# Performance work log

Hardware: AMD Instinct MI355X
Metric: run time of the kernel (lower is better)

Reference implementation:

```python
import jax, jax.numpy as jnp
import numpy as np
import math

B, S, D, H, DQ, DV = 8, 1024, 1024, 16, 64, 64

def _layernorm(x, gamma, beta, eps=1e-5):
    mu = jnp.mean(x, axis=-1, keepdims=True)
    var = jnp.var(x, axis=-1, keepdims=True)
    return (x - mu) * jax.lax.rsqrt(var + eps) * gamma + beta

def setup_inputs() -> dict:
    key = jax.random.key(0)
    ks = jax.random.split(key, 6)
    x = jax.random.normal(ks[0], (B, S, D), dtype=jnp.float32)
    seq_lens = jax.random.randint(ks[1], (B,), 1, S + 1, dtype=jnp.int32)  # min 1 avoids fully-masked rows
    scale = 0.02
    Wq = jax.random.normal(ks[2], (D, H * DQ), dtype=jnp.float32) * scale
    Wkv = jax.random.normal(ks[3], (D, H * (DQ + DV)), dtype=jnp.float32) * scale
    Wo = jax.random.normal(ks[4], (H * DV, D), dtype=jnp.float32) * scale
    return {
        'x': x, 'seq_lens': seq_lens,
        'Wq': Wq, 'bq': jnp.zeros((H * DQ,), jnp.float32),
        'Wkv': Wkv, 'bkv': jnp.zeros((H * (DQ + DV),), jnp.float32),
        'Wo': Wo, 'bo': jnp.zeros((D,), jnp.float32),
        'gamma': jnp.ones((D,), jnp.float32), 'beta': jnp.zeros((D,), jnp.float32),
    }

def reference(x, seq_lens, Wq, bq, Wkv, bkv, Wo, bo, gamma, beta):
    # Decoder self-attention branch: query == key_value sequence.
    resid = x
    xn = _layernorm(x, gamma, beta)
    q = (xn @ Wq + bq).reshape(B, S, H, DQ).transpose(0, 2, 1, 3)      # bhqd
    kv = xn @ Wkv + bkv
    k = kv[..., : H * DQ].reshape(B, S, H, DQ).transpose(0, 2, 1, 3)   # bhkd
    v = kv[..., H * DQ :].reshape(B, S, H, DV).transpose(0, 2, 1, 3)   # bhkd
    scores = jnp.einsum('bhqd,bhkd->bhqk', q, k) / math.sqrt(DQ)
    key_pos = jnp.arange(S)
    pad_mask = key_pos[None, None, None, :] < seq_lens[:, None, None, None]  # [B,1,1,S]
    causal = jnp.tril(jnp.ones((S, S), dtype=bool))[None, None]              # [1,1,S,S]
    mask = pad_mask & causal
    scores = jnp.where(mask, scores, -jnp.inf)
    attn = jax.nn.softmax(scores, axis=-1)
    out = jnp.einsum('bhqk,bhkd->bhqd', attn, v)
    out = out.transpose(0, 2, 1, 3).reshape(B, S, H * DV)
    return out @ Wo + bo + resid
```

## Files before the change

### kernel.cpp

```cpp
#include <hip/hip_runtime.h>
#include <stdint.h>

#define ND 1024

typedef uint16_t u16;
typedef __bf16 bf16_t;
typedef bf16_t bf16x8 __attribute__((ext_vector_type(8)));
typedef float  f32x4  __attribute__((ext_vector_type(4)));
typedef u16    u16x8  __attribute__((ext_vector_type(8)));
typedef u16    u16x4  __attribute__((ext_vector_type(4)));

__device__ __forceinline__ float bf2f(u16 b){
    uint32_t u = ((uint32_t)b) << 16; float f; __builtin_memcpy(&f, &u, 4); return f;
}
__device__ __forceinline__ u16 f2bf(float f){
    uint32_t u; __builtin_memcpy(&u, &f, 4);
    u += 0x7FFFu + ((u >> 16) & 1u);
    return (u16)(u >> 16);
}
__device__ __forceinline__ bool bf_mode(const void* gamma){
    return *reinterpret_cast<const uint32_t*>(gamma) == 0x3F803F80u;
}
__device__ __forceinline__ float loadv(const void* p, int idx, bool bf){
    return bf ? bf2f(reinterpret_cast<const u16*>(p)[idx])
              : reinterpret_cast<const float*>(p)[idx];
}
__device__ __forceinline__ void gload16(const u16* g, u16* l){
    __builtin_amdgcn_global_load_lds(
        (const __attribute__((address_space(1))) void*)g,
        (__attribute__((address_space(3))) void*)l, 16, 0, 0);
}

__global__ __launch_bounds__(256) void k_ln(const void* __restrict__ x,
                                            const void* __restrict__ gamma,
                                            const void* __restrict__ beta,
                                            u16* __restrict__ xn){
    const bool bf = bf_mode(gamma);
    const int lane = threadIdx.x & 63;
    const int row  = blockIdx.x * 4 + (threadIdx.x >> 6);
    const size_t base = (size_t)row * 1024;
    float v[16];
    if (bf){
        const u16* xp = reinterpret_cast<const u16*>(x) + base;
        #pragma unroll
        for (int j = 0; j < 4; j++){
            u16x4 t4 = *reinterpret_cast<const u16x4*>(xp + j*256 + lane*4);
            #pragma unroll
            for (int e = 0; e < 4; e++) v[j*4 + e] = bf2f(t4[e]);
        }
    } else {
        const float* xp = reinterpret_cast<const float*>(x) + base;
        #pragma unroll
        for (int j = 0; j < 4; j++){
            float4 t = *reinterpret_cast<const float4*>(xp + j*256 + lane*4);
            v[j*4+0] = t.x; v[j*4+1] = t.y; v[j*4+2] = t.z; v[j*4+3] = t.w;
        }
    }
    float s1 = 0.f, s2 = 0.f;
    #pragma unroll
    for (int e = 0; e < 16; e++){ s1 += v[e]; s2 += v[e]*v[e]; }
    #pragma unroll
    for (int off = 32; off; off >>= 1){
        s1 += __shfl_xor(s1, off);
        s2 += __shfl_xor(s2, off);
    }
    const float mu  = s1 * (1.0f / ND);
    const float var = s2 * (1.0f / ND) - mu * mu;
    const float rs  = rsqrtf(var + 1e-5f);
    #pragma unroll
    for (int j = 0; j < 4; j++){
        u16x4 o;
        #pragma unroll
        for (int e = 0; e < 4; e++){
            const int col = j*256 + lane*4 + e;
            o[e] = f2bf((v[j*4+e] - mu) * rs * loadv(gamma, col, bf) + loadv(beta, col, bf));
        }
        *reinterpret_cast<u16x4*>(xn + base + j*256 + lane*4) = o;
    }
}

__global__ __launch_bounds__(256) void k_wt(const void* __restrict__ W,
                                            const void* __restrict__ gamma,
                                            u16* __restrict__ WT, int Ncols){
    const bool bf = bf_mode(gamma);
    __shared__ float tile[32][33];
    const int n0 = blockIdx.x * 32, k0 = blockIdx.y * 32;
    const int tx = threadIdx.x & 31, ty = threadIdx.x >> 5;
    #pragma unroll
    for (int r = 0; r < 4; r++){
        int kk = ty + r * 8;
        tile[kk][tx] = loadv(W, (k0 + kk) * Ncols + n0 + tx, bf);
    }
    __syncthreads();
    #pragma unroll
    for (int r = 0; r < 4; r++){
        int nn = ty + r * 8;
        WT[(size_t)(n0 + nn) * 1024 + k0 + tx] = f2bf(tile[tx][nn]);
    }
}

__global__ __launch_bounds__(256) void k_gemmA(const u16* __restrict__ A,
                                               const u16* __restrict__ BT,
                                               const void* __restrict__ bias0,
                                               const void* __restrict__ bias1,
                                               const void* __restrict__ gamma,
                                               u16* __restrict__ Qo, u16* __restrict__ Ko,
                                               u16* __restrict__ Vo){
    const bool bf = bf_mode(gamma);
    __shared__ u16 Al[128 * 64];
    __shared__ u16 Bl[128 * 64];
    const int x8 = blockIdx.x & 7;
    const int r  = blockIdx.x >> 3;
    const int s  = r >> 6;
    const int t  = r & 63;
    const int bm = x8 * 8 + (t & 7);
    const int bn = s * 8 + (t >> 3);
    const int tid = threadIdx.x, lane = tid & 63, w = tid >> 6;
    const int wr = w >> 1, wc = w & 1;
    const int l15 = lane & 15, g = lane >> 4;
    const int xr = (l15 & 7) * 8;
    f32x4 acc[4][4];
    #pragma unroll
    for (int m = 0; m < 4; m++)
        #pragma unroll
        for (int n = 0; n < 4; n++) acc[m][n] = f32x4{0.f, 0.f, 0.f, 0.f};

    const u16* Ag = A  + (size_t)(bm * 128) * 1024;
    const u16* Bg = BT + (size_t)(bn * 128) * 1024;
    const int srow = tid >> 3, sslot = tid & 7;
    const int sswz = (sslot * 8) ^ ((srow & 7) * 8);

    for (int k0 = 0; k0 < 1024; k0 += 64){
        #pragma unroll
        for (int call = 0; call < 4; call++){
            const int row = srow + call * 32;
            const int c   = tid + call * 256;
            gload16(Ag + (size_t)row * 1024 + k0 + sswz, Al + c * 8);
            gload16(Bg + (size_t)row * 1024 + k0 + sswz, Bl + c * 8);
        }
        __syncthreads();
        #pragma unroll
        for (int kc = 0; kc < 2; kc++){
            bf16x8 af[4], bfr[4];
            #pragma unroll
            for (int m = 0; m < 4; m++){
                const int row = wr*64 + m*16 + l15;
                u16x8 t8 = *reinterpret_cast<const u16x8*>(&Al[row*64 + ((kc*32 + g*8) ^ xr)]);
                af[m] = __builtin_bit_cast(bf16x8, t8);
            }
            #pragma unroll
            for (int n = 0; n < 4; n++){
                const int row = wc*64 + n*16 + l15;
                u16x8 t8 = *reinterpret_cast<const u16x8*>(&Bl[row*64 + ((kc*32 + g*8) ^ xr)]);
                bfr[n] = __builtin_bit_cast(bf16x8, t8);
            }
            #pragma unroll
            for (int m = 0; m < 4; m++)
                #pragma unroll
                for (int n = 0; n < 4; n++)
                    acc[m][n] = __builtin_amdgcn_mfma_f32_16x16x32_bf16(af[m], bfr[n], acc[m][n], 0, 0, 0);
        }
        __syncthreads();
    }
    #pragma unroll
    for (int m = 0; m < 4; m++){
        const int grow = bm * 128 + wr * 64 + m * 16 + g * 4;
        #pragma unroll
        for (int n = 0; n < 4; n++){
            const int gcol = bn * 128 + wc * 64 + n * 16 + l15;
            #pragma unroll
            for (int rr4 = 0; rr4 < 4; rr4++){
                float val = acc[m][n][rr4];
                const int rr = grow + rr4;
                const int b = rr >> 10, ss = rr & 1023;
                if (gcol < 1024){
                    int h = gcol >> 6, d = gcol & 63;
                    val = (val + loadv(bias0, gcol, bf)) * 0.18033688011112042f;
                    Qo[((size_t)(b*16 + h) * 1024 + ss) * 64 + d] = f2bf(val);
                } else if (gcol < 2048){
                    int n2 = gcol - 1024, h = n2 >> 6, d = n2 & 63;
                    val += loadv(bias1, n2, bf);
                    Ko[((size_t)(b*16 + h) * 1024 + ss) * 64 + d] = f2bf(val);
                } else {
                    int n3 = gcol - 2048, h = n3 >> 6, d = n3 & 63;
                    val += loadv(bias1, gcol - 1024, bf);
                    Vo[((size_t)(b*16 + h) * 1024 + ss) * 64 + d] = f2bf(val);
                }
            }
        }
    }
}

__global__ __launch_bounds__(256) void k_gemmB(const u16* __restrict__ A,
                                               const u16* __restrict__ BT,
                                               const void* __restrict__ bias0,
                                               const void* __restrict__ xres,
                                               const void* __restrict__ gamma,
                                               float* __restrict__ outf){
    const bool bf = bf_mode(gamma);
    __shared__ u16 Al[128 * 64];
    __shared__ u16 Bl[128 * 64];
    const int x8 = blockIdx.x & 7;
    const int r  = blockIdx.x >> 3;
    const int bm = x8 * 8 + (r & 7);
    const int bn = r >> 3;
    const int tid = threadIdx.x, lane = tid & 63, w = tid >> 6;
    const int wr = w >> 1, wc = w & 1;
    const int l15 = lane & 15, g = lane >> 4;
    const int xr = (l15 & 7) * 8;
    f32x4 acc[4][4];
    #pragma unroll
    for (int m = 0; m < 4; m++)
        #pragma unroll
        for (int n = 0; n < 4; n++) acc[m][n] = f32x4{0.f, 0.f, 0.f, 0.f};

    const u16* Ag = A  + (size_t)(bm * 128) * 1024;
    const u16* Bg = BT + (size_t)(bn * 128) * 1024;
    const int srow = tid >> 3, sslot = tid & 7;
    const int sswz = (sslot * 8) ^ ((srow & 7) * 8);

    for (int k0 = 0; k0 < 1024; k0 += 64){
        #pragma unroll
        for (int call = 0; call < 4; call++){
            const int row = srow + call * 32;
            const int c   = tid + call * 256;
            gload16(Ag + (size_t)row * 1024 + k0 + sswz, Al + c * 8);
            gload16(Bg + (size_t)row * 1024 + k0 + sswz, Bl + c * 8);
        }
        __syncthreads();
        #pragma unroll
        for (int kc = 0; kc < 2; kc++){
            bf16x8 af[4], bfr[4];
            #pragma unroll
            for (int m = 0; m < 4; m++){
                const int row = wr*64 + m*16 + l15;
                u16x8 t8 = *reinterpret_cast<const u16x8*>(&Al[row*64 + ((kc*32 + g*8) ^ xr)]);
                af[m] = __builtin_bit_cast(bf16x8, t8);
            }
            #pragma unroll
            for (int n = 0; n < 4; n++){
                const int row = wc*64 + n*16 + l15;
                u16x8 t8 = *reinterpret_cast<const u16x8*>(&Bl[row*64 + ((kc*32 + g*8) ^ xr)]);
                bfr[n] = __builtin_bit_cast(bf16x8, t8);
            }
            #pragma unroll
            for (int m = 0; m < 4; m++)
                #pragma unroll
                for (int n = 0; n < 4; n++)
                    acc[m][n] = __builtin_amdgcn_mfma_f32_16x16x32_bf16(af[m], bfr[n], acc[m][n], 0, 0, 0);
        }
        __syncthreads();
    }
    #pragma unroll
    for (int m = 0; m < 4; m++){
        const int grow = bm * 128 + wr * 64 + m * 16 + g * 4;
        #pragma unroll
        for (int n = 0; n < 4; n++){
            const int gcol = bn * 128 + wc * 64 + n * 16 + l15;
            #pragma unroll
            for (int rr4 = 0; rr4 < 4; rr4++){
                float val = acc[m][n][rr4];
                const int rr = grow + rr4;
                val += loadv(bias0, gcol, bf);
                val += loadv(xres, (int)((size_t)rr * 1024 + gcol), bf);
                outf[(size_t)rr * 1024 + gcol] = val;
            }
        }
    }
}

__global__ __launch_bounds__(64, 4) void k_attn(const u16* __restrict__ Q,
                                                const u16* __restrict__ K,
                                                const u16* __restrict__ V,
                                                const int* __restrict__ seq_lens,
                                                u16* __restrict__ AO){
    __shared__ u16 Kl0[32 * 64], Kl1[32 * 64];
    __shared__ u16 Vt[64 * 32];
    __shared__ u16 Pl[32 * 32];
    const int bid = blockIdx.x;
    const int qb = 31 - (bid >> 7);
    const int bh = bid & 127;
    const int b = bh >> 4, h = bh & 15;
    const int lane = threadIdx.x;
    const int l15 = lane & 15, g = lane >> 4;
    const int seqlen = seq_lens[b];
    const int nkt = (min(qb * 32 + 31, seqlen - 1) >> 5) + 1;
    const size_t kvbase = (size_t)bh * 1024;

    bf16x8 qa[2][2];
    #pragma unroll
    for (int m = 0; m < 2; m++)
        #pragma unroll
        for (int kc = 0; kc < 2; kc++){
            const u16* qp = Q + (kvbase + qb*32 + m*16 + l15) * 64 + kc*32 + g*8;
            qa[m][kc] = __builtin_bit_cast(bf16x8, *reinterpret_cast<const u16x8*>(qp));
        }

    float m_run[2] = {-3.0e38f, -3.0e38f};
    float l_run[2] = {0.f, 0.f};
    f32x4 oacc[2][4];
    #pragma unroll
    for (int m = 0; m < 2; m++)
        #pragma unroll
        for (int nf = 0; nf < 4; nf++) oacc[m][nf] = f32x4{0.f, 0.f, 0.f, 0.f};

    const int srow8 = lane >> 3, sslot = lane & 7;
    u16x8 vr[4];

    auto stageK = [&](int kt, u16* dst){
        #pragma unroll
        for (int call = 0; call < 4; call++){
            const int row = srow8 + call * 8;
            const int c   = lane + call * 64;
            gload16(K + (kvbase + kt*32 + row) * 64 + ((sslot * 8) ^ ((row & 7) * 8)), dst + c * 8);
        }
    };
    auto vload = [&](int kt){
        #pragma unroll
        for (int j = 0; j < 4; j++){
            const int c = lane + j * 64;
            vr[j] = *reinterpret_cast<const u16x8*>(V + (kvbase + kt*32 + (c >> 3)) * 64 + (c & 7) * 8);
        }
    };
    auto vstore = [&](){
        #pragma unroll
        for (int j = 0; j < 4; j++){
            const int c = lane + j * 64, k = c >> 3, sl = c & 7;
            #pragma unroll
            for (int i = 0; i < 8; i++){
                const int d = sl * 8 + i;
                Vt[d * 32 + (((k >> 3) ^ ((d >> 3) & 3)) * 8) + (k & 7)] = vr[j][i];
            }
        }
    };

    stageK(0, Kl0); vload(0);
    u16* kcur = Kl0; u16* knext = Kl1;

    for (int kt = 0; kt < nkt; kt++){
        asm volatile("s_waitcnt vmcnt(0)" ::: "memory");
        __builtin_amdgcn_sched_barrier(0);
        vstore();
        const bool pre = (kt + 1 < nkt);
        if (pre){ stageK(kt + 1, knext); vload(kt + 1); }

        f32x4 sa[2][2];
        #pragma unroll
        for (int m = 0; m < 2; m++)
            #pragma unroll
            for (int n = 0; n < 2; n++) sa[m][n] = f32x4{0.f, 0.f, 0.f, 0.f};
        #pragma unroll
        for (int kc = 0; kc < 2; kc++){
            bf16x8 kf[2];
            #pragma unroll
            for (int n = 0; n < 2; n++){
                const int row = n*16 + l15;
                u16x8 t = *reinterpret_cast<const u16x8*>(&kcur[row*64 + ((kc*32 + g*8) ^ ((l15 & 7) * 8))]);
                kf[n] = __builtin_bit_cast(bf16x8, t);
            }
            #pragma unroll
            for (int m = 0; m < 2; m++)
                #pragma unroll
                for (int n = 0; n < 2; n++)
                    sa[m][n] = __builtin_amdgcn_mfma_f32_16x16x32_bf16(kf[n], qa[m][kc], sa[m][n], 0, 0, 0);
        }

        #pragma unroll
        for (int m = 0; m < 2; m++){
            const int q = qb*32 + m*16 + l15;
            const int klim = min(q, seqlen - 1);
            float p[8];
            float rm = -3.0e38f;
            #pragma unroll
            for (int n = 0; n < 2; n++)
                #pragma unroll
                for (int r4 = 0; r4 < 4; r4++){
                    const int k = kt*32 + n*16 + g*4 + r4;
                    float sv = sa[m][n][r4];
                    sv = (k <= klim) ? sv : -3.0e38f;
                    p[n*4 + r4] = sv;
                    rm = fmaxf(rm, sv);
                }
            rm = fmaxf(rm, __shfl_xor(rm, 16));
            rm = fmaxf(rm, __shfl_xor(rm, 32));
            const float mnew = fmaxf(m_run[m], rm);
            const float fac  = exp2f(m_run[m] - mnew);
            m_run[m] = mnew;
            float rs = 0.f;
            #pragma unroll
            for (int n = 0; n < 2; n++)
                #pragma unroll
                for (int r4 = 0; r4 < 4; r4++){
                    const float ev = exp2f(p[n*4 + r4] - mnew);
                    rs += ev;
                    const int ql = m*16 + l15;
                    const int k  = n*16 + g*4 + r4;
                    Pl[ql * 32 + (k ^ ((ql & 3) * 8))] = f2bf(ev);
                }
            rs += __shfl_xor(rs, 16);
            rs += __shfl_xor(rs, 32);
            l_run[m] = l_run[m] * fac + rs;
            #pragma unroll
            for (int r4 = 0; r4 < 4; r4++){
                const float facr = __shfl(fac, g*4 + r4, 16);
                #pragma unroll
                for (int nf = 0; nf < 4; nf++) oacc[m][nf][r4] *= facr;
            }
        }

        {
            bf16x8 pa[2], vf[4];
            #pragma unroll
            for (int m = 0; m < 2; m++){
                const int ql = m*16 + l15;
                u16x8 t = *reinterpret_cast<const u16x8*>(&Pl[ql * 32 + ((g ^ (ql & 3)) * 8)]);
                pa[m] = __builtin_bit_cast(bf16x8, t);
            }
            #pragma unroll
            for (int nf = 0; nf < 4; nf++){
                const int dv = nf*16 + l15;
                u16x8 t = *reinterpret_cast<const u16x8*>(&Vt[dv * 32 + ((g ^ ((dv >> 3) & 3)) * 8)]);
                vf[nf] = __builtin_bit_cast(bf16x8, t);
            }
            #pragma unroll
            for (int m = 0; m < 2; m++)
                #pragma unroll
                for (int nf = 0; nf < 4; nf++)
                    oacc[m][nf] = __builtin_amdgcn_mfma_f32_16x16x32_bf16(pa[m], vf[nf], oacc[m][nf], 0, 0, 0);
        }
        u16* tmp = kcur; kcur = knext; knext = tmp;
    }

    #pragma unroll
    for (int m = 0; m < 2; m++)
        #pragma unroll
        for (int r4 = 0; r4 < 4; r4++){
            const float lv  = __shfl(l_run[m], g*4 + r4, 16);
            const float inv = 1.0f / lv;
            const int sg = qb*32 + m*16 + g*4 + r4;
            #pragma unroll
            for (int nf = 0; nf < 4; nf++){
                const int col = h * 64 + nf * 16 + l15;
                AO[((size_t)b * 1024 + sg) * 1024 + col] = f2bf(oacc[m][nf][r4] * inv);
            }
        }
}

extern "C" void kernel_launch(void* const* d_in, const int* in_sizes, int n_in,
                              void* d_out, int out_size, void* d_ws, size_t ws_size,
                              hipStream_t stream){
    const int exp_sizes[10] = {8388608, 8, 1048576, 1024, 2097152, 2048, 1048576, 1024, 1024, 1024};
    if (n_in != 10) return;
    for (int i = 0; i < 10; i++) if (in_sizes[i] != exp_sizes[i]) return;

    const void* x     = d_in[0];
    const int*  slen  = (const int*)d_in[1];
    const void* Wq    = d_in[2];
    const void* bq    = d_in[3];
    const void* Wkv   = d_in[4];
    const void* bkv   = d_in[5];
    const void* Wo    = d_in[6];
    const void* bo    = d_in[7];
    const void* gamma = d_in[8];
    const void* beta  = d_in[9];

    u16* WTqkv = (u16*)d_ws;
    u16* WoT   = WTqkv + (size_t)3072 * 1024;
    u16* xn    = WoT   + (size_t)1024 * 1024;
    u16* Qb    = xn    + (size_t)8192 * 1024;
    u16* Kb    = Qb    + (size_t)8192 * 1024;
    u16* Vb    = Kb    + (size_t)8192 * 1024;
    u16* AOb   = xn;
    const size_t need = ((size_t)3072 + 1024 + 4 * 8192) * 1024 * 2;
    if (ws_size < need) return;

    k_ln<<<2048, 256, 0, stream>>>(x, gamma, beta, xn);
    k_wt<<<dim3(32, 32), 256, 0, stream>>>(Wq,  gamma, WTqkv, 1024);
    k_wt<<<dim3(64, 32), 256, 0, stream>>>(Wkv, gamma, WTqkv + (size_t)1024 * 1024, 2048);
    k_wt<<<dim3(32, 32), 256, 0, stream>>>(Wo,  gamma, WoT, 1024);
    k_gemmA<<<1536, 256, 0, stream>>>(xn, WTqkv, bq, bkv, gamma, Qb, Kb, Vb);
    k_attn<<<4096, 64, 0, stream>>>(Qb, Kb, Vb, slen, AOb);
    k_gemmB<<<512, 256, 0, stream>>>(AOb, WoT, bo, x, gamma, (float*)d_out);
}
```

Baseline: 230.3 us.

## Keep P in registers and read V via LDS transpose loads in attention

Drops the shared-memory round trip for the softmax probabilities: the exponentiated scores now stay in registers as bf16 MFMA operands, and the PV product switches to 16x16x16 MFMAs. V is staged with async global-to-LDS copies into a double buffer, replacing the register load plus scalar transposed stores, and is read back with ds_read_b64_tr_b16 transpose reads. This removes per-element LDS stores and an LDS barrier round trip. In exchange it issues twice as many smaller MFMAs, relies on inline assembly with a manual lgkmcnt wait, and uses more LDS per block.

```diff
diff --git a/kernel.cpp b/kernel.cpp
--- a/kernel.cpp
+++ b/kernel.cpp
@@ -9,6 +9,7 @@
 typedef float  f32x4  __attribute__((ext_vector_type(4)));
 typedef u16    u16x8  __attribute__((ext_vector_type(8)));
 typedef u16    u16x4  __attribute__((ext_vector_type(4)));
+typedef short  s16x4  __attribute__((ext_vector_type(4)));
 
 __device__ __forceinline__ float bf2f(u16 b){
     uint32_t u = ((uint32_t)b) << 16; float f; __builtin_memcpy(&f, &u, 4); return f;
@@ -29,6 +30,16 @@
     __builtin_amdgcn_global_load_lds(
         (const __attribute__((address_space(1))) void*)g,
         (__attribute__((address_space(3))) void*)l, 16, 0, 0);
+}
+__device__ __forceinline__ f32x4 mfma16(u16x4 a, u16x4 b, f32x4 c){
+#if __has_builtin(__builtin_amdgcn_mfma_f32_16x16x16bf16_1k)
+    return __builtin_amdgcn_mfma_f32_16x16x16bf16_1k(
+        __builtin_bit_cast(s16x4, a), __builtin_bit_cast(s16x4, b), c, 0, 0, 0);
+#else
+    f32x4 d = c;
+    asm("v_mfma_f32_16x16x16_bf16 %0, %1, %2, %0" : "+v"(d) : "v"(a), "v"(b));
+    return d;
+#endif
 }
 
 __global__ __launch_bounds__(256) void k_ln(const void* __restrict__ x,
@@ -275,8 +286,7 @@
                                                 const int* __restrict__ seq_lens,
                                                 u16* __restrict__ AO){
     __shared__ u16 Kl0[32 * 64], Kl1[32 * 64];
-    __shared__ u16 Vt[64 * 32];
-    __shared__ u16 Pl[32 * 32];
+    __shared__ u16 Vl0[32 * 64], Vl1[32 * 64];
     const int bid = blockIdx.x;
     const int qb = 31 - (bid >> 7);
     const int bh = bid & 127;
@@ -305,7 +315,6 @@
         for (int nf = 0; nf < 4; nf++) oacc[m][nf] = f32x4{0.f, 0.f, 0.f, 0.f};
 
     const int srow8 = lane >> 3, sslot = lane & 7;
-    u16x8 vr[4];
 
     auto stageK = [&](int kt, u16* dst){
         #pragma unroll
@@ -315,34 +324,26 @@
             gload16(K + (kvbase + kt*32 + row) * 64 + ((sslot * 8) ^ ((row & 7) * 8)), dst + c * 8);
         }
     };
-    auto vload = [&](int kt){
-        #pragma unroll
-        for (int j = 0; j < 4; j++){
-            const int c = lane + j * 64;
-            vr[j] = *reinterpret_cast<const u16x8*>(V + (kvbase + kt*32 + (c >> 3)) * 64 + (c & 7) * 8);
+    auto stageV = [&](int kt, u16* dst){
+        #pragma unroll
+        for (int call = 0; call < 4; call++){
+            const int c = lane + call * 64;
+            const int s = c >> 3;
+            const int k  = (s & 7) * 4 + ((c & 7) >> 1);
+            const int dv = (s >> 3) * 16 + ((c & 7) & 1) * 8;
+            gload16(V + (kvbase + kt*32 + k) * 64 + dv, dst + c * 8);
         }
     };
-    auto vstore = [&](){
-        #pragma unroll
-        for (int j = 0; j < 4; j++){
-            const int c = lane + j * 64, k = c >> 3, sl = c & 7;
-            #pragma unroll
-            for (int i = 0; i < 8; i++){
-                const int d = sl * 8 + i;
-                Vt[d * 32 + (((k >> 3) ^ ((d >> 3) & 3)) * 8) + (k & 7)] = vr[j][i];
-            }
-        }
-    };
-
-    stageK(0, Kl0); vload(0);
+
+    stageK(0, Kl0); stageV(0, Vl0);
     u16* kcur = Kl0; u16* knext = Kl1;
+    u16* vcur = Vl0; u16* vnext = Vl1;
 
     for (int kt = 0; kt < nkt; kt++){
         asm volatile("s_waitcnt vmcnt(0)" ::: "memory");
         __builtin_amdgcn_sched_barrier(0);
-        vstore();
         const bool pre = (kt + 1 < nkt);
-        if (pre){ stageK(kt + 1, knext); vload(kt + 1); }
+        if (pre){ stageK(kt + 1, knext); stageV(kt + 1, vnext); }
 
         f32x4 sa[2][2];
         #pragma unroll
@@ -365,11 +366,12 @@
                     sa[m][n] = __builtin_amdgcn_mfma_f32_16x16x32_bf16(kf[n], qa[m][kc], sa[m][n], 0, 0, 0);
         }
 
+        u16x4 pa[2][2];
         #pragma unroll
         for (int m = 0; m < 2; m++){
             const int q = qb*32 + m*16 + l15;
             const int klim = min(q, seqlen - 1);
-            float p[8];
+            float p[8], pe[8];
             float rm = -3.0e38f;
             #pragma unroll
             for (int n = 0; n < 2; n++)
@@ -388,15 +390,15 @@
             m_run[m] = mnew;
             float rs = 0.f;
             #pragma unroll
-            for (int n = 0; n < 2; n++)
-                #pragma unroll
-                for (int r4 = 0; r4 < 4; r4++){
-                    const float ev = exp2f(p[n*4 + r4] - mnew);
-                    rs += ev;
-                    const int ql = m*16 + l15;
-                    const int k  = n*16 + g*4 + r4;
-                    Pl[ql * 32 + (k ^ ((ql & 3) * 8))] = f2bf(ev);
-                }
+            for (int e = 0; e < 8; e++){
+                pe[e] = exp2f(p[e] - mnew);
+                rs += pe[e];
+            }
+            #pragma unroll
+            for (int j = 0; j < 4; j++){
+                pa[m][0][j] = f2bf(pe[j]);
+                pa[m][1][j] = f2bf(pe[4 + j]);
+            }
             rs += __shfl_xor(rs, 16);
             rs += __shfl_xor(rs, 32);
             l_run[m] = l_run[m] * fac + rs;
@@ -409,28 +411,32 @@
         }
 
         {
-            bf16x8 pa[2], vf[4];
-            #pragma unroll
-            for (int m = 0; m < 2; m++){
-                const int ql = m*16 + l15;
-                u16x8 t = *reinterpret_cast<const u16x8*>(&Pl[ql * 32 + ((g ^ (ql & 3)) * 8)]);
-                pa[m] = __builtin_bit_cast(bf16x8, t);
-            }
-            #pragma unroll
-            for (int nf = 0; nf < 4; nf++){
-                const int dv = nf*16 + l15;
-                u16x8 t = *reinterpret_cast<const u16x8*>(&Vt[dv * 32 + ((g ^ ((dv >> 3) & 3)) * 8)]);
-                vf[nf] = __builtin_bit_cast(bf16x8, t);
-            }
+            const uint32_t vbase =
+                (uint32_t)(uintptr_t)(__attribute__((address_space(3))) u16*)vcur + lane * 8;
+            u16x4 vb[2][4];
+            #pragma unroll
+            for (int kc = 0; kc < 2; kc++)
+                #pragma unroll
+                for (int nf = 0; nf < 4; nf++){
+                    asm volatile("ds_read_b64_tr_b16 %0, %1 offset:%2"
+                                 : "=v"(vb[kc][nf])
+                                 : "v"(vbase), "i"(nf * 1024 + kc * 512));
+                }
+            asm volatile("s_waitcnt lgkmcnt(0)" ::: "memory");
+            __builtin_amdgcn_sched_barrier(0);
             #pragma unroll
             for (int m = 0; m < 2; m++)
                 #pragma unroll
-                for (int nf = 0; nf < 4; nf++)
-                    oacc[m][nf] = __builtin_amdgcn_mfma_f32_16x16x32_bf16(pa[m], vf[nf], oacc[m][nf], 0, 0, 0);
-        }
-        u16* tmp = kcur; kcur = knext; knext = tmp;
-    }
-
+                for (int kc = 0; kc < 2; kc++)
+                    #pragma unroll
+                    for (int nf = 0; nf < 4; nf++)
+                        oacc[m][nf] = mfma16(pa[m][kc], vb[kc][nf], oacc[m][nf]);
+        }
+        u16* tk = kcur; kcur = knext; knext = tk;
+        u16* tv = vcur; vcur = vnext; vnext = tv;
+    }
+
+    asm volatile("s_nop 7\ns_nop 7" :::);
     #pragma unroll
     for (int m = 0; m < 2; m++)
         #pragma unroll
```

Result: faster. 223.4 us (-3.0%).
